# Kernel optimization log

Hardware: AMD Instinct MI355X
Metric: run time of the kernel (lower is better)

Reference implementation:

```python
import jax, jax.numpy as jnp
import numpy as np

N = 20000
NEG_SLOPE = 0.2


def gatv2_layer(x, src, dst, edge_attr, Wl, bl, Wr, br, We, att, bias, H, C):
    """PyG GATv2Conv: add self-loops (edge_attr fill='mean'), gather-score-softmax-aggregate."""
    n = x.shape[0]
    E = src.shape[0]
    # --- add self loops, self-loop edge_attr = mean of incoming edge_attr per node ---
    ea_sum = jax.ops.segment_sum(edge_attr, dst, num_segments=n)
    deg = jax.ops.segment_sum(jnp.ones((E, 1), x.dtype), dst, num_segments=n)
    ea_loop = ea_sum / jnp.maximum(deg, 1.0)
    loop = jnp.arange(n)
    src_a = jnp.concatenate([src, loop])
    dst_a = jnp.concatenate([dst, loop])
    ea = jnp.concatenate([edge_attr, ea_loop], axis=0)
    # --- linear projections ---
    xl = (x @ Wl + bl).reshape(n, H, C)   # source-side features
    xr = (x @ Wr + br).reshape(n, H, C)   # target-side features
    e = (ea @ We).reshape(-1, H, C)       # edge features
    # --- per-edge GATv2 attention score ---
    m = xl[src_a] + xr[dst_a] + e                          # [E', H, C]
    s = jnp.sum(jax.nn.leaky_relu(m, NEG_SLOPE) * att, -1)  # [E', H]
    # --- softmax over incoming edges of each target node ---
    smax = jax.ops.segment_max(s, dst_a, num_segments=n)
    ex = jnp.exp(s - smax[dst_a])
    denom = jax.ops.segment_sum(ex, dst_a, num_segments=n)
    alpha = ex / (denom[dst_a] + 1e-16)                    # [E', H]
    # --- aggregate messages (alpha * x_l[src]) ---
    out = jax.ops.segment_sum(alpha[..., None] * xl[src_a], dst_a, num_segments=n)
    return out.reshape(n, H * C) + bias


def setup_inputs() -> dict:
    key = jax.random.key(0)
    ks = jax.random.split(key, 20)
    F, HID, H1, A = 128, 32, 8, 128
    E = 640000
    d = {}
    d["x"] = jax.random.normal(ks[0], (N, F), jnp.float32)
    d["edge_index"] = jax.random.randint(ks[1], (2, E), 0, N, jnp.int32).astype(jnp.int64)
    d["edge_attr"] = jax.random.normal(ks[2], (E, 1), jnp.float32)
    # layer 1 params (in=F, out=HID, heads=H1)
    d["W1l"] = jax.random.normal(ks[3], (F, H1 * HID), jnp.float32) * 0.05
    d["b1l"] = jnp.zeros((H1 * HID,), jnp.float32)
    d["W1r"] = jax.random.normal(ks[4], (F, H1 * HID), jnp.float32) * 0.05
    d["b1r"] = jnp.zeros((H1 * HID,), jnp.float32)
    d["We1"] = jax.random.normal(ks[5], (1, H1 * HID), jnp.float32) * 0.05
    d["att1"] = jax.random.normal(ks[6], (H1, HID), jnp.float32) * 0.05
    d["bias1"] = jnp.zeros((H1 * HID,), jnp.float32)
    # layer 2 params (in=H1*HID, out=A, heads=1)
    d["W2l"] = jax.random.normal(ks[7], (H1 * HID, A), jnp.float32) * 0.05
    d["b2l"] = jnp.zeros((A,), jnp.float32)
    d["W2r"] = jax.random.normal(ks[8], (H1 * HID, A), jnp.float32) * 0.05
    d["b2r"] = jnp.zeros((A,), jnp.float32)
    d["We2"] = jax.random.normal(ks[9], (1, A), jnp.float32) * 0.05
    d["att2"] = jax.random.normal(ks[10], (1, A), jnp.float32) * 0.05
    d["bias2"] = jnp.zeros((A,), jnp.float32)
    d["alpha"] = jnp.array(0.0, jnp.float32)
    return d


def reference(x, edge_index, edge_attr, W1l, b1l, W1r, b1r, We1, att1, bias1,
              W2l, b2l, W2r, b2r, We2, att2, bias2, alpha):
    src, dst = edge_index[0], edge_index[1]
    h = jax.nn.relu(gatv2_layer(x, src, dst, edge_attr, W1l, b1l, W1r, b1r,
                                We1, att1, bias1, H=8, C=32))
    h = jax.nn.relu(gatv2_layer(h, src, dst, edge_attr, W2l, b2l, W2r, b2r,
                                We2, att2, bias2, H=1, C=128))
    pooled = jnp.mean(h, axis=0, keepdims=True)  # global_mean_pool, single graph -> [1, A]
    return jax.nn.softmax(pooled, axis=1), jax.nn.sigmoid(alpha)
```

## Files before the change

### kernel.cpp

```cpp
#include <hip/hip_runtime.h>
#include <math.h>

#define NEG_SLOPE 0.2f
#define LOG2E 1.4426950408889634f

typedef __attribute__((ext_vector_type(8))) short short8;
typedef __attribute__((ext_vector_type(4))) float f32x4;

__device__ __forceinline__ int imin(int a, int b) { return a < b ? a : b; }

__device__ __forceinline__ unsigned int f2bf(float f) {
    unsigned int u = __float_as_uint(f);
    return (u + 0x7fffu + ((u >> 16) & 1u)) >> 16;
}
__device__ __forceinline__ void bf2f(unsigned int u, float& a, float& b) {
    a = __uint_as_float(u << 16);
    b = __uint_as_float(u & 0xffff0000u);
}
__device__ __forceinline__ float fast_exp2(float x) {
#if __has_builtin(__builtin_amdgcn_exp2f)
    return __builtin_amdgcn_exp2f(x);
#else
    return exp2f(x);
#endif
}
template <int CTRL>
__device__ __forceinline__ float dpp_add(float v) {
    int t = __builtin_amdgcn_update_dpp(0, __float_as_int(v), CTRL, 0xF, 0xF, true);
    return v + __int_as_float(t);
}

__global__ void edge_hist(const int* __restrict__ ei, const float* __restrict__ ea,
                          unsigned long long* __restrict__ hist, int E) {
    int e = blockIdx.x * blockDim.x + threadIdx.x;
    if (e < E) {
        int d = ei[E + e];
        long long fx = (long long)__float2int_rn(ea[e] * 65536.0f);
        unsigned long long v = ((unsigned long long)fx << 32) | 1ull;
        atomicAdd(&hist[(size_t)d * 8], v);
    }
}

__global__ void scan_a(const unsigned long long* __restrict__ hist, int* __restrict__ bsum, int n) {
    __shared__ int wred[4];
    int base = blockIdx.x * 1024;
    int tid = threadIdx.x;
    int s = 0;
#pragma unroll
    for (int k = 0; k < 4; ++k) {
        int i = base + tid + k * 256;
        if (i < n) s += (int)(hist[(size_t)i * 8] & 0xffffffffull);
    }
#pragma unroll
    for (int off = 32; off > 0; off >>= 1) s += __shfl_xor(s, off, 64);
    if ((tid & 63) == 0) wred[tid >> 6] = s;
    __syncthreads();
    if (tid == 0) bsum[blockIdx.x] = wred[0] + wred[1] + wred[2] + wred[3];
}

__global__ void scan_b(int* __restrict__ bsum, int* __restrict__ row_ptr, int B, int n) {
    int tid = threadIdx.x;
    int v = (tid < B) ? bsum[tid] : 0;
    int s = v;
#pragma unroll
    for (int off = 1; off < 64; off <<= 1) {
        int t = __shfl_up(s, off, 64);
        if (tid >= off) s += t;
    }
    if (tid < B) bsum[tid] = s - v;
    if (tid == 63) row_ptr[n] = s;
}

__global__ void scan_c(const unsigned long long* __restrict__ hist,
                       const int* __restrict__ bsum, int* __restrict__ row_ptr,
                       int* __restrict__ wptr_pad, float* __restrict__ ea_loop, int n) {
    __shared__ int wtot[4];
    int tid = threadIdx.x;
    int wid = tid >> 6, lane = tid & 63;
    int i0 = blockIdx.x * 1024 + tid * 4;
    int dcnt[4]; float esum[4];
#pragma unroll
    for (int k = 0; k < 4; ++k) {
        if (i0 + k < n) {
            unsigned long long h = hist[(size_t)(i0 + k) * 8];
            dcnt[k] = (int)(h & 0xffffffffull);
            esum[k] = (float)((int)(h >> 32)) * (1.0f / 65536.0f);
        } else { dcnt[k] = 0; esum[k] = 0.0f; }
    }
    int tsum = dcnt[0] + dcnt[1] + dcnt[2] + dcnt[3];
    int s = tsum;
#pragma unroll
    for (int off = 1; off < 64; off <<= 1) {
        int t = __shfl_up(s, off, 64);
        if (lane >= off) s += t;
    }
    if (lane == 63) wtot[wid] = s;
    __syncthreads();
    int wpre = 0;
#pragma unroll
    for (int k = 0; k < 4; ++k) if (k < wid) wpre += wtot[k];
    int pre = bsum[blockIdx.x] + wpre + (s - tsum);
    if (i0 < n) {
        int4 e;
        e.x = pre;
        e.y = pre + dcnt[0];
        e.z = e.y + dcnt[1];
        e.w = e.z + dcnt[2];
        *(int4*)(row_ptr + i0) = e;
        int ev[4] = { e.x, e.y, e.z, e.w };
        float4 el;
        el.x = esum[0] / fmaxf((float)dcnt[0], 1.0f);
        el.y = esum[1] / fmaxf((float)dcnt[1], 1.0f);
        el.z = esum[2] / fmaxf((float)dcnt[2], 1.0f);
        el.w = esum[3] / fmaxf((float)dcnt[3], 1.0f);
        *(float4*)(ea_loop + i0) = el;
#pragma unroll
        for (int k = 0; k < 4; ++k) wptr_pad[(size_t)(i0 + k) * 16] = ev[k];
    }
}

__global__ void edge_scatter(const int* __restrict__ ei, const float* __restrict__ ea,
                             int* __restrict__ wptr_pad, int2* __restrict__ spk, int E) {
    int e = blockIdx.x * blockDim.x + threadIdx.x;
    if (e < E) {
        int d = ei[E + e];
        int pos = atomicAdd(&wptr_pad[(size_t)d * 16], 1);
        spk[pos] = make_int2(ei[e], __float_as_int(ea[e]));
    }
}

__global__ void cvt_bf16_v4(const float* __restrict__ in, unsigned short* __restrict__ out, int sz4) {
    int i = blockIdx.x * blockDim.x + threadIdx.x;
    if (i < sz4) {
        float4 v = ((const float4*)in)[i];
        uint2 r;
        r.x = f2bf(v.x) | (f2bf(v.y) << 16);
        r.y = f2bf(v.z) | (f2bf(v.w) << 16);
        ((uint2*)out)[i] = r;
    }
}

__global__ void prep_weights(const float* __restrict__ W1l, const float* __restrict__ W1r,
                             const float* __restrict__ W2l, const float* __restrict__ W2r,
                             const float* __restrict__ b1l, const float* __restrict__ b1r,
                             const float* __restrict__ b2l, const float* __restrict__ b2r,
                             unsigned short* __restrict__ Wt1, unsigned short* __restrict__ Wt2,
                             float* __restrict__ b1cat, float* __restrict__ b2cat,
                             int F, int HC1, int HC2) {
    int S1 = F * HC1, S2 = HC1 * HC2;
    int i = blockIdx.x * blockDim.x + threadIdx.x;
    if (i < S1) {
        int k = i / HC1, nn = i - k * HC1;
        Wt1[(size_t)nn * F + k] = (unsigned short)f2bf(W1l[i]);
    } else if (i < 2 * S1) {
        int j = i - S1;
        int k = j / HC1, nn = j - k * HC1;
        Wt1[(size_t)(HC1 + nn) * F + k] = (unsigned short)f2bf(W1r[j]);
    } else if (i < 2 * S1 + S2) {
        int j = i - 2 * S1;
        int k = j / HC2, nn = j - k * HC2;
        Wt2[(size_t)nn * HC1 + k] = (unsigned short)f2bf(W2l[j]);
    } else if (i < 2 * S1 + 2 * S2) {
        int j = i - 2 * S1 - S2;
        int k = j / HC2, nn = j - k * HC2;
        Wt2[(size_t)(HC2 + nn) * HC1 + k] = (unsigned short)f2bf(W2r[j]);
    } else if (i < 2 * S1 + 2 * S2 + 2 * HC1) {
        int j = i - 2 * S1 - 2 * S2;
        b1cat[j] = (j < HC1) ? b1l[j] : b1r[j - HC1];
    } else if (i < 2 * S1 + 2 * S2 + 2 * HC1 + 2 * HC2) {
        int j = i - 2 * S1 - 2 * S2 - 2 * HC1;
        b2cat[j] = (j < HC2) ? b2l[j] : b2r[j - HC2];
    }
}

__global__ void __launch_bounds__(256)
gemm_bf16(const unsigned short* __restrict__ A, const unsigned short* __restrict__ Bt,
          const float* __restrict__ bias, unsigned short* __restrict__ C,
          int M, int N, int K) {
    __shared__ __attribute__((aligned(16))) unsigned short As[64 * 40];
    __shared__ __attribute__((aligned(16))) unsigned short Bs[64 * 40];
    int tid  = threadIdx.x;
    int wave = tid >> 6, lane = tid & 63;
    int m0 = blockIdx.x * 64, n0 = blockIdx.y * 64;
    int row = tid >> 2, kg = (tid & 3) * 8;

    f32x4 acc[4] = {};
    for (int kk = 0; kk < K; kk += 32) {
        int gm = m0 + row;
        uint4 av;
        if (gm < M) av = *(const uint4*)(A + (size_t)gm * K + kk + kg);
        else        av = make_uint4(0, 0, 0, 0);
        *(uint4*)&As[row * 40 + kg] = av;
        uint4 bv = *(const uint4*)(Bt + (size_t)(n0 + row) * K + kk + kg);
        *(uint4*)&Bs[row * 40 + kg] = bv;
        __syncthreads();
        short8 a = *(const short8*)&As[(wave * 16 + (lane & 15)) * 40 + (lane >> 4) * 8];
#pragma unroll
        for (int g = 0; g < 4; ++g) {
            short8 b = *(const short8*)&Bs[(g * 16 + (lane & 15)) * 40 + (lane >> 4) * 8];
            acc[g] = __builtin_amdgcn_mfma_f32_16x16x32_bf16(a, b, acc[g], 0, 0, 0);
        }
        __syncthreads();
    }
#pragma unroll
    for (int g = 0; g < 4; ++g) {
        int col = n0 + g * 16 + (lane & 15);
        float bs = bias[col];
#pragma unroll
        for (int r = 0; r < 4; ++r) {
            int grow = m0 + wave * 16 + (lane >> 4) * 4 + r;
            if (grow < M) C[(size_t)grow * N + col] = (unsigned short)f2bf(acc[g][r] + bs);
        }
    }
}

template <int NV>
__device__ __forceinline__ void ld_row(float* r, const float* p) {
    if constexpr (NV == 4) {
        float4 t = *(const float4*)p;
        r[0] = t.x; r[1] = t.y; r[2] = t.z; r[3] = t.w;
    } else {
        float2 t = *(const float2*)p;
        r[0] = t.x; r[1] = t.y;
    }
}
template <int NV>
__device__ __forceinline__ uint2 ld_bf(const unsigned short* __restrict__ base, int laneoff) {
    uint2 r;
    if constexpr (NV == 4) r = *(const uint2*)(base + laneoff);
    else { r.x = *(const unsigned int*)(base + laneoff); r.y = 0; }
    return r;
}
template <int G>
__device__ __forceinline__ float grp_reduce(float vs) {
    vs = dpp_add<0xB1>(vs);
    vs = dpp_add<0x4E>(vs);
    vs = dpp_add<0x141>(vs);
    if constexpr (G >= 16) vs = dpp_add<0x140>(vs);
    if constexpr (G >= 32) {
        int t = __builtin_amdgcn_ds_swizzle(__float_as_int(vs), 0x401F);
        vs += __int_as_float(t);
    }
    if constexpr (G >= 64) vs += __shfl_xor(vs, 32, 64);
    return vs;
}

template <int HC, int STRIDE, int C, bool OUT_BF16>
__global__ void __launch_bounds__(256, 4)
gat_agg(const unsigned short* __restrict__ xlr,
        const float* __restrict__ We, const float* __restrict__ att,
        const float* __restrict__ bias,
        const int* __restrict__ row_ptr, const int2* __restrict__ spk,
        const float* __restrict__ ea_loop,
        void* __restrict__ out, int n) {
    constexpr int NV = HC / 64;
    constexpr int G  = C / NV;
    int wave = threadIdx.x >> 6;
    int lane = threadIdx.x & 63;
    int node = blockIdx.x * 4 + wave;
    if (node >= n) return;
    int laneoff = lane * NV;

    float xr_r[NV], We_r[NV], att6[NV], att4[NV], o[NV];
    {
        uint2 u = ld_bf<NV>(xlr + (size_t)node * STRIDE + HC, laneoff);
        bf2f(u.x, xr_r[0], xr_r[1]);
        if constexpr (NV == 4) bf2f(u.y, xr_r[2], xr_r[3]);
    }
    ld_row<NV>(We_r, We + laneoff);
    {
        float att_r[NV];
        ld_row<NV>(att_r, att + laneoff);
#pragma unroll
        for (int j = 0; j < NV; ++j) {
            att6[j] = 0.6f * LOG2E * att_r[j];
            att4[j] = 0.4f * LOG2E * att_r[j];
        }
    }
#pragma unroll
    for (int j = 0; j < NV; ++j) o[j] = 0.0f;

    int start = __builtin_amdgcn_readfirstlane(row_ptr[node]);
    int end   = __builtin_amdgcn_readfirstlane(row_ptr[node + 1]);
    float ea_l = ea_loop[node];
    float l = 0.0f;

    auto process = [&](uint2 xu, float w) {
        float xf[NV];
        bf2f(xu.x, xf[0], xf[1]);
        if constexpr (NV == 4) bf2f(xu.y, xf[2], xf[3]);
        float vs = 0.0f;
#pragma unroll
        for (int j = 0; j < NV; ++j) {
            float mm = xf[j] + fmaf(w, We_r[j], xr_r[j]);
            vs = fmaf(att6[j], mm, vs);
            vs = fmaf(att4[j], fabsf(mm), vs);
        }
        vs = grp_reduce<G>(vs);
        float pr = fast_exp2(vs);
        l += pr;
#pragma unroll
        for (int j = 0; j < NV; ++j) o[j] = fmaf(pr, xf[j], o[j]);
    };

    process(ld_bf<NV>(xlr + (size_t)node * STRIDE, laneoff), ea_l);

    int cnt = end - start;
    for (int b0 = 0; b0 < cnt; b0 += 64) {
        int rem = imin(64, cnt - b0);
        int idx = start + b0 + lane;
        int idxc = imin(idx, end - 1);
        int2 pv = spk[idxc];

        auto rl = [&](int j) {
            int s = __builtin_amdgcn_readlane(pv.x, j);
            return ld_bf<NV>(xlr + (size_t)s * STRIDE, laneoff);
        };
        auto rw = [&](int j) {
            return __int_as_float(__builtin_amdgcn_readlane(pv.y, j));
        };

        int rc = rem - 1;
        uint2 X0 = rl(0),            X1 = rl(imin(1, rc)),
              X2 = rl(imin(2, rc)),  X3 = rl(imin(3, rc));
        float W0 = rw(0),            W1 = rw(imin(1, rc)),
              W2 = rw(imin(2, rc)),  W3 = rw(imin(3, rc));

        int j = 0;
        for (; j + 4 <= rem; j += 4) {
            uint2 Y0 = rl(imin(j + 4, rc)), Y1 = rl(imin(j + 5, rc)),
                  Y2 = rl(imin(j + 6, rc)), Y3 = rl(imin(j + 7, rc));
            float U0 = rw(imin(j + 4, rc)), U1 = rw(imin(j + 5, rc)),
                  U2 = rw(imin(j + 6, rc)), U3 = rw(imin(j + 7, rc));
            process(X0, W0); process(X1, W1); process(X2, W2); process(X3, W3);
            X0 = Y0; X1 = Y1; X2 = Y2; X3 = Y3;
            W0 = U0; W1 = U1; W2 = U2; W3 = U3;
        }
        if (j < rem) {
            process(X0, W0);
            if (j + 1 < rem) {
                process(X1, W1);
                if (j + 2 < rem) process(X2, W2);
            }
        }
    }

    float inv = 1.0f / (l + 1e-16f);
    float b_r[NV];
    ld_row<NV>(b_r, bias + laneoff);
    float v[NV];
#pragma unroll
    for (int j = 0; j < NV; ++j) v[j] = fmaxf(o[j] * inv + b_r[j], 0.0f);

    if constexpr (OUT_BF16) {
        unsigned short* op = (unsigned short*)out + (size_t)node * HC + laneoff;
        if constexpr (NV == 4) {
            uint2 t;
            t.x = f2bf(v[0]) | (f2bf(v[1]) << 16);
            t.y = f2bf(v[2]) | (f2bf(v[3]) << 16);
            *(uint2*)op = t;
        } else {
            *(unsigned int*)op = f2bf(v[0]) | (f2bf(v[1]) << 16);
        }
    } else {
        float* op = (float*)out + (size_t)node * HC + laneoff;
        if constexpr (NV == 4) { *(float4*)op = make_float4(v[0], v[1], v[2], v[3]); }
        else                   { *(float2*)op = make_float2(v[0], v[1]); }
    }
}

__global__ void pool_partial(const float* __restrict__ h2, float* __restrict__ partial, int n) {
    int t = threadIdx.x;
    float s = 0.0f;
    for (int r = blockIdx.x; r < n; r += gridDim.x) s += h2[(size_t)r * 128 + t];
    partial[blockIdx.x * 128 + t] = s;
}

__global__ void __launch_bounds__(1024)
pool_final(const float* __restrict__ partial, int nb,
           const float* __restrict__ alpha_in,
           float* __restrict__ out, int n) {
    __shared__ float acc[8][128];
    __shared__ float red[4];
    int t = threadIdx.x & 127;
    int g = threadIdx.x >> 7;
    float s = 0.0f;
    for (int b = g; b < nb; b += 8) s += partial[b * 128 + t];
    acc[g][t] = s;
    __syncthreads();
    if (threadIdx.x < 128) {
        float tot = 0.0f;
#pragma unroll
        for (int k = 0; k < 8; ++k) tot += acc[k][t];
        float mean = tot / (float)n;
        float mx = mean;
#pragma unroll
        for (int off = 32; off > 0; off >>= 1) mx = fmaxf(mx, __shfl_xor(mx, off, 64));
        if ((t & 63) == 0) red[t >> 6] = mx;
        __syncthreads();
        mx = fmaxf(red[0], red[1]);
        float ex = __expf(mean - mx);
        float sm = ex;
#pragma unroll
        for (int off = 32; off > 0; off >>= 1) sm += __shfl_xor(sm, off, 64);
        if ((t & 63) == 0) red[2 + (t >> 6)] = sm;
        __syncthreads();
        sm = red[2] + red[3];
        out[t] = ex / sm;
        if (t == 0) out[128] = 1.0f / (1.0f + __expf(-alpha_in[0]));
    }
}

extern "C" void kernel_launch(void* const* d_in, const int* in_sizes, int n_in,
                              void* d_out, int out_size, void* d_ws, size_t ws_size,
                              hipStream_t stream) {
    const float* x    = (const float*)d_in[0];
    const int*   ei   = (const int*)d_in[1];
    const float* ea   = (const float*)d_in[2];
    const float* W1l  = (const float*)d_in[3];
    const float* b1l  = (const float*)d_in[4];
    const float* W1r  = (const float*)d_in[5];
    const float* b1r  = (const float*)d_in[6];
    const float* We1  = (const float*)d_in[7];
    const float* att1 = (const float*)d_in[8];
    const float* bias1= (const float*)d_in[9];
    const float* W2l  = (const float*)d_in[10];
    const float* b2l  = (const float*)d_in[11];
    const float* W2r  = (const float*)d_in[12];
    const float* b2r  = (const float*)d_in[13];
    const float* We2  = (const float*)d_in[14];
    const float* att2 = (const float*)d_in[15];
    const float* bias2= (const float*)d_in[16];
    const float* alpha= (const float*)d_in[17];
    float* out = (float*)d_out;

    const int F = 128, HC1 = 256, HC2 = 128;
    const int n = in_sizes[0] / F;
    const int E = in_sizes[1] / 2;
    const int B = (n + 1023) / 1024;

    char* ws = (char*)d_ws;
    size_t off = 0;
    auto alloc = [&](size_t bytes) { size_t p = off; off += (bytes + 255) & ~(size_t)255; return p; };

    unsigned long long* hist = (unsigned long long*)(ws + alloc((size_t)n * 8 * 8));
    int*   row_ptr = (int*)  (ws + alloc((size_t)(n + 1) * 4));
    int*   wptr    = (int*)  (ws + alloc((size_t)n * 16 * 4));
    float* ea_loop = (float*)(ws + alloc((size_t)n * 4));
    int*   bsum    = (int*)  (ws + alloc(64 * 4));
    int2*  spk     = (int2*) (ws + alloc((size_t)E * 8));
    unsigned short* xb   = (unsigned short*)(ws + alloc((size_t)n * F * 2));
    unsigned short* Wt1  = (unsigned short*)(ws + alloc((size_t)F * (2 * HC1) * 2));
    unsigned short* Wt2  = (unsigned short*)(ws + alloc((size_t)HC1 * (2 * HC2) * 2));
    float* b1cat   = (float*)(ws + alloc((size_t)2 * HC1 * 4));
    float* b2cat   = (float*)(ws + alloc((size_t)2 * HC2 * 4));
    unsigned short* xlr1 = (unsigned short*)(ws + alloc((size_t)n * 2 * HC1 * 2));
    unsigned short* h1   = (unsigned short*)(ws + alloc((size_t)n * HC1 * 2));
    float* h2      = (float*)(ws + alloc((size_t)n * HC2 * 4));
    float* partial = (float*)(ws + alloc((size_t)256 * 128 * 4));
    unsigned short* xlr2 = xlr1;
    const int NB_POOL = 256;

    (void)hipMemsetAsync(hist, 0, (size_t)n * 8 * 8, stream);

    int tb = 256;
    edge_hist<<<(E + tb - 1) / tb, tb, 0, stream>>>(ei, ea, hist, E);
    scan_a<<<B, 256, 0, stream>>>(hist, bsum, n);
    scan_b<<<1, 64, 0, stream>>>(bsum, row_ptr, B, n);
    scan_c<<<B, 256, 0, stream>>>(hist, bsum, row_ptr, wptr, ea_loop, n);
    edge_scatter<<<(E + tb - 1) / tb, tb, 0, stream>>>(ei, ea, wptr, spk, E);

    cvt_bf16_v4<<<(n * F / 4 + tb - 1) / tb, tb, 0, stream>>>(x, xb, n * F / 4);
    {
        int total = 2 * F * HC1 + 2 * HC1 * HC2 + 2 * HC1 + 2 * HC2;
        prep_weights<<<(total + tb - 1) / tb, tb, 0, stream>>>(
            W1l, W1r, W2l, W2r, b1l, b1r, b2l, b2r, Wt1, Wt2, b1cat, b2cat, F, HC1, HC2);
    }

    {
        dim3 grid((n + 63) / 64, (2 * HC1) / 64);
        gemm_bf16<<<grid, 256, 0, stream>>>(xb, Wt1, b1cat, xlr1, n, 2 * HC1, F);
    }
    gat_agg<256, 512, 32, true><<<(n + 3) / 4, 256, 0, stream>>>(
        xlr1, We1, att1, bias1, row_ptr, spk, ea_loop, h1, n);

    {
        dim3 grid((n + 63) / 64, (2 * HC2) / 64);
        gemm_bf16<<<grid, 256, 0, stream>>>(h1, Wt2, b2cat, xlr2, n, 2 * HC2, HC1);
    }
    gat_agg<128, 256, 128, false><<<(n + 3) / 4, 256, 0, stream>>>(
        xlr2, We2, att2, bias2, row_ptr, spk, ea_loop, h2, n);

    pool_partial<<<NB_POOL, 128, 0, stream>>>(h2, partial, n);
    pool_final<<<1, 1024, 0, stream>>>(partial, NB_POOL, alpha, out, n);
}
```

Baseline: 312.1 us.

## Store projected node features in fp8, fuse prep kernels and pooling

The GEMM outputs (xl/xr for both layers) are now written as fp8 instead of bf16, which halves the bytes gathered per edge in the aggregation kernels. The edge histogram, x-to-bf16 conversion and weight transposition are merged into one launch. The layer-2 output is no longer written to memory: it is atomically accumulated into 256 pooling slots, which removes the h2 buffer and the pool_partial kernel. The launch_bounds occupancy hint is also dropped. This trades accuracy (fp8 features with a small mantissa) for memory traffic, and the slot atomics may contend.

```diff
diff --git a/kernel.cpp b/kernel.cpp
--- a/kernel.cpp
+++ b/kernel.cpp
@@ -6,6 +6,7 @@
 
 typedef __attribute__((ext_vector_type(8))) short short8;
 typedef __attribute__((ext_vector_type(4))) float f32x4;
+typedef __attribute__((ext_vector_type(2))) float v2f;
 
 __device__ __forceinline__ int imin(int a, int b) { return a < b ? a : b; }
 
@@ -24,20 +25,65 @@
     return exp2f(x);
 #endif
 }
+__device__ __forceinline__ unsigned char f2fp8(float v) {
+    return (unsigned char)(__builtin_amdgcn_cvt_pk_fp8_f32(v, v, 0, false) & 0xff);
+}
 template <int CTRL>
 __device__ __forceinline__ float dpp_add(float v) {
     int t = __builtin_amdgcn_update_dpp(0, __float_as_int(v), CTRL, 0xF, 0xF, true);
     return v + __int_as_float(t);
 }
 
-__global__ void edge_hist(const int* __restrict__ ei, const float* __restrict__ ea,
-                          unsigned long long* __restrict__ hist, int E) {
-    int e = blockIdx.x * blockDim.x + threadIdx.x;
-    if (e < E) {
-        int d = ei[E + e];
-        long long fx = (long long)__float2int_rn(ea[e] * 65536.0f);
+__global__ void fused_prep(const int* __restrict__ ei, const float* __restrict__ ea,
+                           unsigned long long* __restrict__ hist, int E,
+                           const float* __restrict__ x, unsigned short* __restrict__ xb, int nF4,
+                           const float* __restrict__ W1l, const float* __restrict__ W1r,
+                           const float* __restrict__ W2l, const float* __restrict__ W2r,
+                           const float* __restrict__ b1l, const float* __restrict__ b1r,
+                           const float* __restrict__ b2l, const float* __restrict__ b2r,
+                           unsigned short* __restrict__ Wt1, unsigned short* __restrict__ Wt2,
+                           float* __restrict__ b1cat, float* __restrict__ b2cat,
+                           int F, int HC1, int HC2) {
+    int i = blockIdx.x * blockDim.x + threadIdx.x;
+    if (i < E) {
+        int d = ei[E + i];
+        long long fx = (long long)__float2int_rn(ea[i] * 65536.0f);
         unsigned long long v = ((unsigned long long)fx << 32) | 1ull;
         atomicAdd(&hist[(size_t)d * 8], v);
+        return;
+    }
+    int j = i - E;
+    if (j < nF4) {
+        float4 v = ((const float4*)x)[j];
+        uint2 r;
+        r.x = f2bf(v.x) | (f2bf(v.y) << 16);
+        r.y = f2bf(v.z) | (f2bf(v.w) << 16);
+        ((uint2*)xb)[j] = r;
+        return;
+    }
+    int k = j - nF4;
+    int S1 = F * HC1, S2 = HC1 * HC2;
+    if (k < S1) {
+        int kk = k / HC1, nn = k - kk * HC1;
+        Wt1[(size_t)nn * F + kk] = (unsigned short)f2bf(W1l[k]);
+    } else if (k < 2 * S1) {
+        int m = k - S1;
+        int kk = m / HC1, nn = m - kk * HC1;
+        Wt1[(size_t)(HC1 + nn) * F + kk] = (unsigned short)f2bf(W1r[m]);
+    } else if (k < 2 * S1 + S2) {
+        int m = k - 2 * S1;
+        int kk = m / HC2, nn = m - kk * HC2;
+        Wt2[(size_t)nn * HC1 + kk] = (unsigned short)f2bf(W2l[m]);
+    } else if (k < 2 * S1 + 2 * S2) {
+        int m = k - 2 * S1 - S2;
+        int kk = m / HC2, nn = m - kk * HC2;
+        Wt2[(size_t)(HC2 + nn) * HC1 + kk] = (unsigned short)f2bf(W2r[m]);
+    } else if (k < 2 * S1 + 2 * S2 + 2 * HC1) {
+        int m = k - 2 * S1 - 2 * S2;
+        b1cat[m] = (m < HC1) ? b1l[m] : b1r[m - HC1];
+    } else if (k < 2 * S1 + 2 * S2 + 2 * HC1 + 2 * HC2) {
+        int m = k - 2 * S1 - 2 * S2 - 2 * HC1;
+        b2cat[m] = (m < HC2) ? b2l[m] : b2r[m - HC2];
     }
 }
 
@@ -129,53 +175,10 @@
     }
 }
 
-__global__ void cvt_bf16_v4(const float* __restrict__ in, unsigned short* __restrict__ out, int sz4) {
-    int i = blockIdx.x * blockDim.x + threadIdx.x;
-    if (i < sz4) {
-        float4 v = ((const float4*)in)[i];
-        uint2 r;
-        r.x = f2bf(v.x) | (f2bf(v.y) << 16);
-        r.y = f2bf(v.z) | (f2bf(v.w) << 16);
-        ((uint2*)out)[i] = r;
-    }
-}
-
-__global__ void prep_weights(const float* __restrict__ W1l, const float* __restrict__ W1r,
-                             const float* __restrict__ W2l, const float* __restrict__ W2r,
-                             const float* __restrict__ b1l, const float* __restrict__ b1r,
-                             const float* __restrict__ b2l, const float* __restrict__ b2r,
-                             unsigned short* __restrict__ Wt1, unsigned short* __restrict__ Wt2,
-                             float* __restrict__ b1cat, float* __restrict__ b2cat,
-                             int F, int HC1, int HC2) {
-    int S1 = F * HC1, S2 = HC1 * HC2;
-    int i = blockIdx.x * blockDim.x + threadIdx.x;
-    if (i < S1) {
-        int k = i / HC1, nn = i - k * HC1;
-        Wt1[(size_t)nn * F + k] = (unsigned short)f2bf(W1l[i]);
-    } else if (i < 2 * S1) {
-        int j = i - S1;
-        int k = j / HC1, nn = j - k * HC1;
-        Wt1[(size_t)(HC1 + nn) * F + k] = (unsigned short)f2bf(W1r[j]);
-    } else if (i < 2 * S1 + S2) {
-        int j = i - 2 * S1;
-        int k = j / HC2, nn = j - k * HC2;
-        Wt2[(size_t)nn * HC1 + k] = (unsigned short)f2bf(W2l[j]);
-    } else if (i < 2 * S1 + 2 * S2) {
-        int j = i - 2 * S1 - S2;
-        int k = j / HC2, nn = j - k * HC2;
-        Wt2[(size_t)(HC2 + nn) * HC1 + k] = (unsigned short)f2bf(W2r[j]);
-    } else if (i < 2 * S1 + 2 * S2 + 2 * HC1) {
-        int j = i - 2 * S1 - 2 * S2;
-        b1cat[j] = (j < HC1) ? b1l[j] : b1r[j - HC1];
-    } else if (i < 2 * S1 + 2 * S2 + 2 * HC1 + 2 * HC2) {
-        int j = i - 2 * S1 - 2 * S2 - 2 * HC1;
-        b2cat[j] = (j < HC2) ? b2l[j] : b2r[j - HC2];
-    }
-}
-
+template <bool OUT_FP8>
 __global__ void __launch_bounds__(256)
 gemm_bf16(const unsigned short* __restrict__ A, const unsigned short* __restrict__ Bt,
-          const float* __restrict__ bias, unsigned short* __restrict__ C,
+          const float* __restrict__ bias, void* __restrict__ Cv,
           int M, int N, int K) {
     __shared__ __attribute__((aligned(16))) unsigned short As[64 * 40];
     __shared__ __attribute__((aligned(16))) unsigned short Bs[64 * 40];
@@ -209,7 +212,14 @@
 #pragma unroll
         for (int r = 0; r < 4; ++r) {
             int grow = m0 + wave * 16 + (lane >> 4) * 4 + r;
-            if (grow < M) C[(size_t)grow * N + col] = (unsigned short)f2bf(acc[g][r] + bs);
+            if (grow < M) {
+                float val = acc[g][r] + bs;
+                if constexpr (OUT_FP8) {
+                    ((unsigned char*)Cv)[(size_t)grow * N + col] = f2fp8(val);
+                } else {
+                    ((unsigned short*)Cv)[(size_t)grow * N + col] = (unsigned short)f2bf(val);
+                }
+            }
         }
     }
 }
@@ -225,11 +235,18 @@
     }
 }
 template <int NV>
-__device__ __forceinline__ uint2 ld_bf(const unsigned short* __restrict__ base, int laneoff) {
-    uint2 r;
-    if constexpr (NV == 4) r = *(const uint2*)(base + laneoff);
-    else { r.x = *(const unsigned int*)(base + laneoff); r.y = 0; }
-    return r;
+__device__ __forceinline__ unsigned int ld_fp8(const unsigned char* __restrict__ base, int off) {
+    if constexpr (NV == 4) return *(const unsigned int*)(base + off);
+    else                   return (unsigned int)(*(const unsigned short*)(base + off));
+}
+template <int NV>
+__device__ __forceinline__ void unp_fp8(unsigned int u, float* xf) {
+    v2f p0 = __builtin_amdgcn_cvt_pk_f32_fp8(u, false);
+    xf[0] = p0.x; xf[1] = p0.y;
+    if constexpr (NV == 4) {
+        v2f p1 = __builtin_amdgcn_cvt_pk_f32_fp8(u, true);
+        xf[2] = p1.x; xf[3] = p1.y;
+    }
 }
 template <int G>
 __device__ __forceinline__ float grp_reduce(float vs) {
@@ -245,9 +262,9 @@
     return vs;
 }
 
-template <int HC, int STRIDE, int C, bool OUT_BF16>
-__global__ void __launch_bounds__(256, 4)
-gat_agg(const unsigned short* __restrict__ xlr,
+template <int HC, int STRIDE, int C, int OUT_MODE>
+__global__ void __launch_bounds__(256)
+gat_agg(const unsigned char* __restrict__ xlr,
         const float* __restrict__ We, const float* __restrict__ att,
         const float* __restrict__ bias,
         const int* __restrict__ row_ptr, const int2* __restrict__ spk,
@@ -262,11 +279,7 @@
     int laneoff = lane * NV;
 
     float xr_r[NV], We_r[NV], att6[NV], att4[NV], o[NV];
-    {
-        uint2 u = ld_bf<NV>(xlr + (size_t)node * STRIDE + HC, laneoff);
-        bf2f(u.x, xr_r[0], xr_r[1]);
-        if constexpr (NV == 4) bf2f(u.y, xr_r[2], xr_r[3]);
-    }
+    unp_fp8<NV>(ld_fp8<NV>(xlr + (size_t)node * STRIDE + HC, laneoff), xr_r);
     ld_row<NV>(We_r, We + laneoff);
     {
         float att_r[NV];
@@ -285,10 +298,9 @@
     float ea_l = ea_loop[node];
     float l = 0.0f;
 
-    auto process = [&](uint2 xu, float w) {
+    auto process = [&](unsigned int xu, float w) {
         float xf[NV];
-        bf2f(xu.x, xf[0], xf[1]);
-        if constexpr (NV == 4) bf2f(xu.y, xf[2], xf[3]);
+        unp_fp8<NV>(xu, xf);
         float vs = 0.0f;
 #pragma unroll
         for (int j = 0; j < NV; ++j) {
@@ -303,7 +315,7 @@
         for (int j = 0; j < NV; ++j) o[j] = fmaf(pr, xf[j], o[j]);
     };
 
-    process(ld_bf<NV>(xlr + (size_t)node * STRIDE, laneoff), ea_l);
+    process(ld_fp8<NV>(xlr + (size_t)node * STRIDE, laneoff), ea_l);
 
     int cnt = end - start;
     for (int b0 = 0; b0 < cnt; b0 += 64) {
@@ -314,22 +326,22 @@
 
         auto rl = [&](int j) {
             int s = __builtin_amdgcn_readlane(pv.x, j);
-            return ld_bf<NV>(xlr + (size_t)s * STRIDE, laneoff);
+            return ld_fp8<NV>(xlr + (size_t)s * STRIDE, laneoff);
         };
         auto rw = [&](int j) {
             return __int_as_float(__builtin_amdgcn_readlane(pv.y, j));
         };
 
         int rc = rem - 1;
-        uint2 X0 = rl(0),            X1 = rl(imin(1, rc)),
-              X2 = rl(imin(2, rc)),  X3 = rl(imin(3, rc));
+        unsigned int X0 = rl(0),           X1 = rl(imin(1, rc)),
+                     X2 = rl(imin(2, rc)), X3 = rl(imin(3, rc));
         float W0 = rw(0),            W1 = rw(imin(1, rc)),
               W2 = rw(imin(2, rc)),  W3 = rw(imin(3, rc));
 
         int j = 0;
         for (; j + 4 <= rem; j += 4) {
-            uint2 Y0 = rl(imin(j + 4, rc)), Y1 = rl(imin(j + 5, rc)),
-                  Y2 = rl(imin(j + 6, rc)), Y3 = rl(imin(j + 7, rc));
+            unsigned int Y0 = rl(imin(j + 4, rc)), Y1 = rl(imin(j + 5, rc)),
+                         Y2 = rl(imin(j + 6, rc)), Y3 = rl(imin(j + 7, rc));
             float U0 = rw(imin(j + 4, rc)), U1 = rw(imin(j + 5, rc)),
                   U2 = rw(imin(j + 6, rc)), U3 = rw(imin(j + 7, rc));
             process(X0, W0); process(X1, W1); process(X2, W2); process(X3, W3);
@@ -352,7 +364,7 @@
 #pragma unroll
     for (int j = 0; j < NV; ++j) v[j] = fmaxf(o[j] * inv + b_r[j], 0.0f);
 
-    if constexpr (OUT_BF16) {
+    if constexpr (OUT_MODE == 0) {
         unsigned short* op = (unsigned short*)out + (size_t)node * HC + laneoff;
         if constexpr (NV == 4) {
             uint2 t;
@@ -363,17 +375,10 @@
             *(unsigned int*)op = f2bf(v[0]) | (f2bf(v[1]) << 16);
         }
     } else {
-        float* op = (float*)out + (size_t)node * HC + laneoff;
-        if constexpr (NV == 4) { *(float4*)op = make_float4(v[0], v[1], v[2], v[3]); }
-        else                   { *(float2*)op = make_float2(v[0], v[1]); }
-    }
-}
-
-__global__ void pool_partial(const float* __restrict__ h2, float* __restrict__ partial, int n) {
-    int t = threadIdx.x;
-    float s = 0.0f;
-    for (int r = blockIdx.x; r < n; r += gridDim.x) s += h2[(size_t)r * 128 + t];
-    partial[blockIdx.x * 128 + t] = s;
+        float* pacc = (float*)out + (size_t)(blockIdx.x & 255) * 128 + laneoff;
+#pragma unroll
+        for (int j = 0; j < NV; ++j) atomicAdd(&pacc[j], v[j]);
+    }
 }
 
 __global__ void __launch_bounds__(1024)
@@ -454,43 +459,43 @@
     unsigned short* Wt2  = (unsigned short*)(ws + alloc((size_t)HC1 * (2 * HC2) * 2));
     float* b1cat   = (float*)(ws + alloc((size_t)2 * HC1 * 4));
     float* b2cat   = (float*)(ws + alloc((size_t)2 * HC2 * 4));
-    unsigned short* xlr1 = (unsigned short*)(ws + alloc((size_t)n * 2 * HC1 * 2));
-    unsigned short* h1   = (unsigned short*)(ws + alloc((size_t)n * HC1 * 2));
-    float* h2      = (float*)(ws + alloc((size_t)n * HC2 * 4));
+    unsigned char* xlr1 = (unsigned char*)(ws + alloc((size_t)n * 2 * HC1));
+    unsigned short* h1  = (unsigned short*)(ws + alloc((size_t)n * HC1 * 2));
     float* partial = (float*)(ws + alloc((size_t)256 * 128 * 4));
-    unsigned short* xlr2 = xlr1;
-    const int NB_POOL = 256;
+    unsigned char* xlr2 = xlr1;
+    const int NB_SLOTS = 256;
 
     (void)hipMemsetAsync(hist, 0, (size_t)n * 8 * 8, stream);
+    (void)hipMemsetAsync(partial, 0, (size_t)NB_SLOTS * 128 * 4, stream);
 
     int tb = 256;
-    edge_hist<<<(E + tb - 1) / tb, tb, 0, stream>>>(ei, ea, hist, E);
+    {
+        int nF4  = n * F / 4;
+        int WTOT = 2 * F * HC1 + 2 * HC1 * HC2 + 2 * HC1 + 2 * HC2;
+        int total = E + nF4 + WTOT;
+        fused_prep<<<(total + tb - 1) / tb, tb, 0, stream>>>(
+            ei, ea, hist, E, x, xb, nF4,
+            W1l, W1r, W2l, W2r, b1l, b1r, b2l, b2r,
+            Wt1, Wt2, b1cat, b2cat, F, HC1, HC2);
+    }
     scan_a<<<B, 256, 0, stream>>>(hist, bsum, n);
     scan_b<<<1, 64, 0, stream>>>(bsum, row_ptr, B, n);
     scan_c<<<B, 256, 0, stream>>>(hist, bsum, row_ptr, wptr, ea_loop, n);
     edge_scatter<<<(E + tb - 1) / tb, tb, 0, stream>>>(ei, ea, wptr, spk, E);
 
-    cvt_bf16_v4<<<(n * F / 4 + tb - 1) / tb, tb, 0, stream>>>(x, xb, n * F / 4);
-    {
-        int total = 2 * F * HC1 + 2 * HC1 * HC2 + 2 * HC1 + 2 * HC2;
-        prep_weights<<<(total + tb - 1) / tb, tb, 0, stream>>>(
-            W1l, W1r, W2l, W2r, b1l, b1r, b2l, b2r, Wt1, Wt2, b1cat, b2cat, F, HC1, HC2);
-    }
-
     {
         dim3 grid((n + 63) / 64, (2 * HC1) / 64);
-        gemm_bf16<<<grid, 256, 0, stream>>>(xb, Wt1, b1cat, xlr1, n, 2 * HC1, F);
-    }
-    gat_agg<256, 512, 32, true><<<(n + 3) / 4, 256, 0, stream>>>(
+        gemm_bf16<true><<<grid, 256, 0, stream>>>(xb, Wt1, b1cat, xlr1, n, 2 * HC1, F);
+    }
+    gat_agg<256, 512, 32, 0><<<(n + 3) / 4, 256, 0, stream>>>(
         xlr1, We1, att1, bias1, row_ptr, spk, ea_loop, h1, n);
 
     {
         dim3 grid((n + 63) / 64, (2 * HC2) / 64);
-        gemm_bf16<<<grid, 256, 0, stream>>>(h1, Wt2, b2cat, xlr2, n, 2 * HC2, HC1);
-    }
-    gat_agg<128, 256, 128, false><<<(n + 3) / 4, 256, 0, stream>>>(
-        xlr2, We2, att2, bias2, row_ptr, spk, ea_loop, h2, n);
-
-    pool_partial<<<NB_POOL, 128, 0, stream>>>(h2, partial, n);
-    pool_final<<<1, 1024, 0, stream>>>(partial, NB_POOL, alpha, out, n);
-}
+        gemm_bf16<true><<<grid, 256, 0, stream>>>(h1, Wt2, b2cat, xlr2, n, 2 * HC2, HC1);
+    }
+    gat_agg<128, 256, 128, 1><<<(n + 3) / 4, 256, 0, stream>>>(
+        xlr2, We2, att2, bias2, row_ptr, spk, ea_loop, partial, n);
+
+    pool_final<<<1, 1024, 0, stream>>>(partial, NB_SLOTS, alpha, out, n);
+}
```

Result: faster. 279.6 us (-10.4%).
